# Optimization experiments

Hardware: AMD Instinct MI355X
Metric: run time of the kernel (lower is better)

## Reference

```python
import jax, jax.numpy as jnp
import numpy as np

B, L, D, DH = 4, 2048, 1024, 2048

def setup_inputs() -> dict:
    key = jax.random.key(0)
    ks = jax.random.split(key, 9)
    return {
        "x": jax.random.normal(ks[0], (B, L, D), jnp.float32),
        "W_in": jax.random.normal(ks[1], (DH, D), jnp.float32) / np.sqrt(D).astype(np.float32),
        "b_in": jnp.zeros((DH,), jnp.float32),
        "W_out": jax.random.normal(ks[2], (D, DH), jnp.float32) / np.sqrt(DH).astype(np.float32),
        "b_out": jnp.zeros((D,), jnp.float32),
        "phazor": jax.random.normal(ks[3], (DH, 2), jnp.float32),
        "phazor_init": jax.random.normal(ks[4], (DH, 2), jnp.float32),
        "last_conv_re": jax.random.normal(ks[5], (B, DH), jnp.float32),
        "last_conv_im": jax.random.normal(ks[6], (B, DH), jnp.float32),
    }

def reference(x, W_in, b_in, W_out, b_out, phazor, phazor_init, last_conv_re, last_conv_im):
    batch, length, _ = x.shape
    # linear_in, cast to float32 (already fp32 here)
    h = x @ W_in.T + b_in                                  # [B, L, DH]
    # view_as_complex of [DH, 2] params
    p = phazor[:, 0] + 1j * phazor[:, 1]                   # [DH]
    p0 = phazor_init[:, 0] + 1j * phazor_init[:, 1]        # [DH]
    pa = jnp.abs(p)
    p = p / pa * jnp.exp(-pa)                              # unit phase, exp(-|p|) magnitude
    # phazor_progression[t, c] = p[c] ** t
    prog = p[None, :] ** jnp.arange(length)[:, None]       # [L, DH] complex
    filt = prog * p0[None, :]                              # [L, DH]
    # FFT convolution with zero padding to 2L (linear convolution)
    ff = jnp.fft.fft(filt, n=2 * length, axis=0)           # [2L, DH]
    xf = jnp.fft.fft(h, n=2 * length, axis=1)              # [B, 2L, DH]
    conv = jnp.fft.ifft(ff[None] * xf, axis=1)[:, :length] # [B, L, DH]
    # add decayed contribution of past state (detached state)
    last = last_conv_re + 1j * last_conv_im                # [B, DH]
    conv_with_past = conv + last[:, None, :] * prog[None] * p[None, None, :]
    y = jax.nn.silu(conv_with_past.real)                   # back to real dtype
    return y @ W_out.T + b_out                             # [B, L, D]
```

## Files before the change

### kernel.cpp

```cpp
#include <hip/hip_runtime.h>
#include <math.h>

#define WS_B  4
#define WS_L  2048
#define WS_D  1024
#define WS_DH 2048
#define WS_M  (WS_B * WS_L)
#define NCH   32
#define CHUNK (WS_L / NCH)

typedef __attribute__((ext_vector_type(4))) float     f32x4;
typedef _Float16 f16x8 __attribute__((ext_vector_type(8)));
typedef _Float16 f16x4 __attribute__((ext_vector_type(4)));

#define GLDS(gptr, lptr) \
    __builtin_amdgcn_global_load_lds( \
        (const __attribute__((address_space(1))) unsigned int*)(gptr), \
        (__attribute__((address_space(3))) unsigned int*)(lptr), 16, 0, 0)

__global__ void pack_f16(const float* __restrict__ src, _Float16* __restrict__ dst,
                         int K, int k8log, int nChunks) {
    int chunk = blockIdx.x * 256 + threadIdx.x;
    if (chunk >= nChunks) return;
    int r    = chunk & 127;
    int rest = chunk >> 7;
    int K8m  = (1 << k8log) - 1;
    int kc   = rest & K8m;
    int rb   = rest >> k8log;
    const float* s = src + ((size_t)(rb * 128 + r) * K + kc * 8);
    f32x4 v0 = *(const f32x4*)s;
    f32x4 v1 = *(const f32x4*)(s + 4);
    f16x8 h;
#pragma unroll
    for (int k = 0; k < 4; ++k) { h[k] = (_Float16)v0[k]; h[4 + k] = (_Float16)v1[k]; }
    *(f16x8*)(dst + (size_t)chunk * 8) = h;
}

template<int K8, int LDC, typename OutT>
__global__ __launch_bounds__(256, 4)
void gemm_f16_packed(const _Float16* __restrict__ A, const _Float16* __restrict__ B,
                     const float* __restrict__ bias, OutT* __restrict__ C)
{
    __shared__ alignas(16) _Float16 sA[2][4][128][8];
    __shared__ alignas(16) _Float16 sB[2][4][128][8];

    const int tid  = threadIdx.x;
    const int lane = tid & 63;
    const int wave = tid >> 6;
    const int wm   = (wave >> 1) * 64;
    const int wn   = (wave & 1) * 64;
    const int m15  = lane & 15;
    const int q    = lane >> 4;

    const int bm = blockIdx.x;
    const int bn = blockIdx.y;

    f32x4 acc[4][4] = {};

    auto stage = [&](int kc0, int buf) {
#pragma unroll
        for (int i = 0; i < 2; ++i) {
            int c   = i * 256 + tid;
            int row = c & 127;
            int kq  = c >> 7;
            size_t ac = ((size_t)(bm * K8 + kc0 + kq) * 128 + row) * 8;
            size_t bc = ((size_t)(bn * K8 + kc0 + kq) * 128 + row) * 8;
            GLDS(A + ac, &sA[buf][kq][row][0]);
            GLDS(B + bc, &sB[buf][kq][row][0]);
        }
    };

    stage(0, 0);
    int buf = 0;
    for (int kc0 = 0; kc0 < K8; kc0 += 4, buf ^= 1) {
        __syncthreads();
        if (kc0 + 4 < K8) stage(kc0 + 4, buf ^ 1);

        f16x8 af[4], bf[4];
#pragma unroll
        for (int i = 0; i < 4; ++i) {
            af[i] = *(const f16x8*)&sA[buf][q][wm + i * 16 + m15][0];
            bf[i] = *(const f16x8*)&sB[buf][q][wn + i * 16 + m15][0];
        }
#pragma unroll
        for (int i = 0; i < 4; ++i)
#pragma unroll
            for (int j = 0; j < 4; ++j)
                acc[i][j] = __builtin_amdgcn_mfma_f32_16x16x32_f16(af[i], bf[j], acc[i][j], 0, 0, 0);
    }

    const int r4 = (lane >> 4) * 4;
#pragma unroll
    for (int j = 0; j < 4; ++j) {
        int col = bn * 128 + wn + j * 16 + m15;
        float bv = bias[col];
#pragma unroll
        for (int i = 0; i < 4; ++i) {
            int row0 = bm * 128 + wm + i * 16 + r4;
#pragma unroll
            for (int r = 0; r < 4; ++r)
                C[(size_t)(row0 + r) * LDC + col] = (OutT)(acc[i][j][r] + bv);
        }
    }
}

__device__ inline void compute_p(const float* __restrict__ phazor, int c, float& pre, float& pim) {
    float zr = phazor[2 * c], zi = phazor[2 * c + 1];
    float pa = sqrtf(zr * zr + zi * zi);
    float sc = expf(-pa) / pa;
    pre = zr * sc;
    pim = zi * sc;
}

__global__ void scan_local(const _Float16* __restrict__ h, const float* __restrict__ phazor,
                           const float* __restrict__ phazor_init, float* __restrict__ Uend) {
    int idx = blockIdx.x * blockDim.x + threadIdx.x;
    if (idx >= WS_B * NCH * WS_DH) return;
    int c  = idx & (WS_DH - 1);
    int bj = idx >> 11;
    int j  = bj & (NCH - 1);
    int b  = bj >> 5;
    float pre, pim;
    compute_p(phazor, c, pre, pim);
    float p0r = phazor_init[2 * c], p0i = phazor_init[2 * c + 1];
    const _Float16* hp = h + ((size_t)(b * WS_L + j * CHUNK)) * WS_DH + c;
    float ur = 0.f, ui = 0.f;
    for (int t = 0; t < CHUNK; t += 8) {
        float hv[8];
#pragma unroll
        for (int u = 0; u < 8; ++u) hv[u] = (float)hp[(size_t)(t + u) * WS_DH];
#pragma unroll
        for (int u = 0; u < 8; ++u) {
            float nr = fmaf(pre, ur, fmaf(-pim, ui, p0r * hv[u]));
            float ni = fmaf(pre, ui, fmaf( pim, ur, p0i * hv[u]));
            ur = nr; ui = ni;
        }
    }
    Uend[2 * idx] = ur;
    Uend[2 * idx + 1] = ui;
}

__global__ void scan_carry(const float* __restrict__ Uend, float* __restrict__ carry,
                           const float* __restrict__ phazor,
                           const float* __restrict__ last_re, const float* __restrict__ last_im) {
    int idx = blockIdx.x * blockDim.x + threadIdx.x;
    if (idx >= WS_B * WS_DH) return;
    int c = idx & (WS_DH - 1);
    int b = idx >> 11;
    float pre, pim;
    compute_p(phazor, c, pre, pim);
    float qr = pre, qi = pim;
#pragma unroll
    for (int s = 0; s < 6; ++s) {
        float nr = qr * qr - qi * qi;
        qi = 2.f * qr * qi;
        qr = nr;
    }
    float ur = last_re[idx], ui = last_im[idx];
    for (int j = 0; j < NCH; ++j) {
        int o = (b * NCH + j) * WS_DH + c;
        carry[2 * o] = ur;
        carry[2 * o + 1] = ui;
        float Lr = Uend[2 * o], Li = Uend[2 * o + 1];
        float nr = fmaf(qr, ur, fmaf(-qi, ui, Lr));
        float ni = fmaf(qr, ui, fmaf( qi, ur, Li));
        ur = nr; ui = ni;
    }
}

__global__ void scan_apply(const _Float16* __restrict__ h, const float* __restrict__ phazor,
                           const float* __restrict__ phazor_init, const float* __restrict__ carry,
                           _Float16* __restrict__ yh) {
    int idx = blockIdx.x * blockDim.x + threadIdx.x;
    if (idx >= WS_B * NCH * WS_DH) return;
    int c  = idx & (WS_DH - 1);
    int bj = idx >> 11;
    int j  = bj & (NCH - 1);
    int b  = bj >> 5;
    float pre, pim;
    compute_p(phazor, c, pre, pim);
    float p0r = phazor_init[2 * c], p0i = phazor_init[2 * c + 1];
    float ur = carry[2 * idx], ui = carry[2 * idx + 1];
    const int row0 = b * WS_L + j * CHUNK;
    const _Float16* hp = h + (size_t)row0 * WS_DH + c;
    const int chi = c >> 3, clo = c & 7;
    for (int t = 0; t < CHUNK; t += 8) {
        float hv[8];
#pragma unroll
        for (int u = 0; u < 8; ++u) hv[u] = (float)hp[(size_t)(t + u) * WS_DH];
#pragma unroll
        for (int u = 0; u < 8; ++u) {
            float nr = fmaf(pre, ur, fmaf(-pim, ui, p0r * hv[u]));
            float ni = fmaf(pre, ui, fmaf( pim, ur, p0i * hv[u]));
            ur = nr; ui = ni;
            float z  = ur;
            float yv = z / (1.f + expf(-z));
            int row = row0 + t + u;
            size_t o = (((size_t)(row >> 7) * 256 + chi) * 128 + (row & 127)) * 8 + clo;
            yh[o] = (_Float16)yv;
        }
    }
}

extern "C" void kernel_launch(void* const* d_in, const int* in_sizes, int n_in,
                              void* d_out, int out_size, void* d_ws, size_t ws_size,
                              hipStream_t stream)
{
    const float* x       = (const float*)d_in[0];
    const float* W_in    = (const float*)d_in[1];
    const float* b_in    = (const float*)d_in[2];
    const float* W_out   = (const float*)d_in[3];
    const float* b_out   = (const float*)d_in[4];
    const float* phazor  = (const float*)d_in[5];
    const float* ph_init = (const float*)d_in[6];
    const float* last_re = (const float*)d_in[7];
    const float* last_im = (const float*)d_in[8];
    float* out = (float*)d_out;

    char* ws = (char*)d_ws;
    size_t off = 0;
    auto alloc = [&](size_t bytes) {
        char* p = ws + off;
        off += (bytes + 255) & ~(size_t)255;
        return p;
    };
    _Float16* xp    = (_Float16*)alloc((size_t)WS_M * WS_D * 2);
    _Float16* w1p   = (_Float16*)alloc((size_t)WS_DH * WS_D * 2);
    _Float16* w2p   = (_Float16*)alloc((size_t)WS_D * WS_DH * 2);
    _Float16* h     = (_Float16*)alloc((size_t)WS_M * WS_DH * 2);
    _Float16* yhp   = (_Float16*)alloc((size_t)WS_M * WS_DH * 2);
    float*    Uend  = (float*)alloc((size_t)WS_B * NCH * WS_DH * 2 * 4);
    float*    carry = (float*)alloc((size_t)WS_B * NCH * WS_DH * 2 * 4);

    {
        int n = WS_M * WS_D / 8;
        pack_f16<<<dim3((n + 255) / 256), dim3(256), 0, stream>>>(x, xp, WS_D, 7, n);
        n = WS_DH * WS_D / 8;
        pack_f16<<<dim3((n + 255) / 256), dim3(256), 0, stream>>>(W_in, w1p, WS_D, 7, n);
        n = WS_D * WS_DH / 8;
        pack_f16<<<dim3((n + 255) / 256), dim3(256), 0, stream>>>(W_out, w2p, WS_DH, 8, n);
    }

    {
        dim3 g(WS_M / 128, WS_DH / 128);
        gemm_f16_packed<WS_D / 8, WS_DH, _Float16><<<g, dim3(256), 0, stream>>>(xp, w1p, b_in, h);
    }

    {
        int total = WS_B * NCH * WS_DH;
        scan_local<<<dim3(total / 256), dim3(256), 0, stream>>>(h, phazor, ph_init, Uend);
        scan_carry<<<dim3(WS_B * WS_DH / 256), dim3(256), 0, stream>>>(Uend, carry, phazor,
                                                                       last_re, last_im);
        scan_apply<<<dim3(total / 256), dim3(256), 0, stream>>>(h, phazor, ph_init, carry, yhp);
    }

    {
        dim3 g(WS_M / 128, WS_D / 128);
        gemm_f16_packed<WS_DH / 8, WS_D, float><<<g, dim3(256), 0, stream>>>(yhp, w2p, b_out, out);
    }
}
```

Measured before the change: 245.8 us.

## Vectorize scan over 8 channels, coalesce packing via LDS, deepen second GEMM K-tile

The scan kernels now handle 8 adjacent channels per thread with 16-byte loads and stores, and use 128 chunks instead of 32. The carry step's power-of-p loop and stores are adjusted to match. pack_f16 stages a 128x128 tile through LDS so that global reads are coalesced. The output GEMM uses a K-stage of 8 with a min-blocks hint of 2. The intent is to remove the strided 2-byte accesses in the scan and the uncoalesced packing reads, at the cost of more registers and a longer sequential carry loop.

```diff
diff --git a/kernel.cpp b/kernel.cpp
--- a/kernel.cpp
+++ b/kernel.cpp
@@ -6,8 +6,9 @@
 #define WS_D  1024
 #define WS_DH 2048
 #define WS_M  (WS_B * WS_L)
-#define NCH   32
+#define NCH   128
 #define CHUNK (WS_L / NCH)
+#define CB    8
 
 typedef __attribute__((ext_vector_type(4))) float     f32x4;
 typedef _Float16 f16x8 __attribute__((ext_vector_type(8)));
@@ -18,31 +19,45 @@
         (const __attribute__((address_space(1))) unsigned int*)(gptr), \
         (__attribute__((address_space(3))) unsigned int*)(lptr), 16, 0, 0)
 
-__global__ void pack_f16(const float* __restrict__ src, _Float16* __restrict__ dst,
-                         int K, int k8log, int nChunks) {
-    int chunk = blockIdx.x * 256 + threadIdx.x;
-    if (chunk >= nChunks) return;
-    int r    = chunk & 127;
-    int rest = chunk >> 7;
-    int K8m  = (1 << k8log) - 1;
-    int kc   = rest & K8m;
-    int rb   = rest >> k8log;
-    const float* s = src + ((size_t)(rb * 128 + r) * K + kc * 8);
-    f32x4 v0 = *(const f32x4*)s;
-    f32x4 v1 = *(const f32x4*)(s + 4);
-    f16x8 h;
-#pragma unroll
-    for (int k = 0; k < 4; ++k) { h[k] = (_Float16)v0[k]; h[4 + k] = (_Float16)v1[k]; }
-    *(f16x8*)(dst + (size_t)chunk * 8) = h;
-}
-
-template<int K8, int LDC, typename OutT>
-__global__ __launch_bounds__(256, 4)
+__global__ __launch_bounds__(256)
+void pack_f16(const float* __restrict__ src, _Float16* __restrict__ dst, int K) {
+    __shared__ alignas(16) _Float16 sT[128][136];
+    const int tid = threadIdx.x;
+    const int rb  = blockIdx.x;
+    const int kb  = blockIdx.y;
+    const int K8  = K >> 3;
+
+#pragma unroll
+    for (int it = 0; it < 16; ++it) {
+        int f    = it * 256 + tid;
+        int row  = f >> 5;
+        int col  = (f & 31) * 4;
+        f32x4 v  = *(const f32x4*)(src + (size_t)(rb * 128 + row) * K + kb * 128 + col);
+        f16x4 hv;
+#pragma unroll
+        for (int k = 0; k < 4; ++k) hv[k] = (_Float16)v[k];
+        *(f16x4*)&sT[row][col] = hv;
+    }
+    __syncthreads();
+
+#pragma unroll
+    for (int it = 0; it < 8; ++it) {
+        int c2 = it * 256 + tid;
+        int r  = c2 & 127;
+        int kq = c2 >> 7;
+        f16x8 hv = *(const f16x8*)&sT[r][kq * 8];
+        size_t chunk = ((size_t)rb * K8 + kb * 16 + kq) * 128 + r;
+        *(f16x8*)(dst + chunk * 8) = hv;
+    }
+}
+
+template<int K8, int LDC, int KQ, int MINB, typename OutT>
+__global__ __launch_bounds__(256, MINB)
 void gemm_f16_packed(const _Float16* __restrict__ A, const _Float16* __restrict__ B,
                      const float* __restrict__ bias, OutT* __restrict__ C)
 {
-    __shared__ alignas(16) _Float16 sA[2][4][128][8];
-    __shared__ alignas(16) _Float16 sB[2][4][128][8];
+    __shared__ alignas(16) _Float16 sA[2][KQ][128][8];
+    __shared__ alignas(16) _Float16 sB[2][KQ][128][8];
 
     const int tid  = threadIdx.x;
     const int lane = tid & 63;
@@ -59,7 +74,7 @@
 
     auto stage = [&](int kc0, int buf) {
 #pragma unroll
-        for (int i = 0; i < 2; ++i) {
+        for (int i = 0; i < KQ / 2; ++i) {
             int c   = i * 256 + tid;
             int row = c & 127;
             int kq  = c >> 7;
@@ -72,21 +87,24 @@
 
     stage(0, 0);
     int buf = 0;
-    for (int kc0 = 0; kc0 < K8; kc0 += 4, buf ^= 1) {
+    for (int kc0 = 0; kc0 < K8; kc0 += KQ, buf ^= 1) {
         __syncthreads();
-        if (kc0 + 4 < K8) stage(kc0 + 4, buf ^ 1);
-
-        f16x8 af[4], bf[4];
-#pragma unroll
-        for (int i = 0; i < 4; ++i) {
-            af[i] = *(const f16x8*)&sA[buf][q][wm + i * 16 + m15][0];
-            bf[i] = *(const f16x8*)&sB[buf][q][wn + i * 16 + m15][0];
-        }
-#pragma unroll
-        for (int i = 0; i < 4; ++i)
-#pragma unroll
-            for (int j = 0; j < 4; ++j)
-                acc[i][j] = __builtin_amdgcn_mfma_f32_16x16x32_f16(af[i], bf[j], acc[i][j], 0, 0, 0);
+        if (kc0 + KQ < K8) stage(kc0 + KQ, buf ^ 1);
+
+#pragma unroll
+        for (int kk = 0; kk < KQ / 4; ++kk) {
+            f16x8 af[4], bf[4];
+#pragma unroll
+            for (int i = 0; i < 4; ++i) {
+                af[i] = *(const f16x8*)&sA[buf][kk * 4 + q][wm + i * 16 + m15][0];
+                bf[i] = *(const f16x8*)&sB[buf][kk * 4 + q][wn + i * 16 + m15][0];
+            }
+#pragma unroll
+            for (int i = 0; i < 4; ++i)
+#pragma unroll
+                for (int j = 0; j < 4; ++j)
+                    acc[i][j] = __builtin_amdgcn_mfma_f32_16x16x32_f16(af[i], bf[j], acc[i][j], 0, 0, 0);
+        }
     }
 
     const int r4 = (lane >> 4) * 4;
@@ -115,29 +133,35 @@
 __global__ void scan_local(const _Float16* __restrict__ h, const float* __restrict__ phazor,
                            const float* __restrict__ phazor_init, float* __restrict__ Uend) {
     int idx = blockIdx.x * blockDim.x + threadIdx.x;
-    if (idx >= WS_B * NCH * WS_DH) return;
-    int c  = idx & (WS_DH - 1);
-    int bj = idx >> 11;
-    int j  = bj & (NCH - 1);
-    int b  = bj >> 5;
-    float pre, pim;
-    compute_p(phazor, c, pre, pim);
-    float p0r = phazor_init[2 * c], p0i = phazor_init[2 * c + 1];
-    const _Float16* hp = h + ((size_t)(b * WS_L + j * CHUNK)) * WS_DH + c;
-    float ur = 0.f, ui = 0.f;
-    for (int t = 0; t < CHUNK; t += 8) {
-        float hv[8];
-#pragma unroll
-        for (int u = 0; u < 8; ++u) hv[u] = (float)hp[(size_t)(t + u) * WS_DH];
-#pragma unroll
-        for (int u = 0; u < 8; ++u) {
-            float nr = fmaf(pre, ur, fmaf(-pim, ui, p0r * hv[u]));
-            float ni = fmaf(pre, ui, fmaf( pim, ur, p0i * hv[u]));
-            ur = nr; ui = ni;
-        }
-    }
-    Uend[2 * idx] = ur;
-    Uend[2 * idx + 1] = ui;
+    int cb   = idx & (WS_DH / CB - 1);
+    int rest = idx >> 8;
+    int j    = rest & (NCH - 1);
+    int b    = rest >> 7;
+    int c0   = cb * CB;
+    float pre[CB], pim[CB], p0r[CB], p0i[CB], ur[CB] = {}, ui[CB] = {};
+#pragma unroll
+    for (int u = 0; u < CB; ++u) {
+        compute_p(phazor, c0 + u, pre[u], pim[u]);
+        p0r[u] = phazor_init[2 * (c0 + u)];
+        p0i[u] = phazor_init[2 * (c0 + u) + 1];
+    }
+    const int row0 = b * WS_L + j * CHUNK;
+    const _Float16* hp = h + (size_t)row0 * WS_DH + c0;
+#pragma unroll
+    for (int t = 0; t < CHUNK; ++t) {
+        f16x8 v = *(const f16x8*)(hp + (size_t)t * WS_DH);
+#pragma unroll
+        for (int u = 0; u < CB; ++u) {
+            float hv = (float)v[u];
+            float nr = fmaf(pre[u], ur[u], fmaf(-pim[u], ui[u], p0r[u] * hv));
+            float ni = fmaf(pre[u], ui[u], fmaf( pim[u], ur[u], p0i[u] * hv));
+            ur[u] = nr; ui[u] = ni;
+        }
+    }
+    float2* Ue = (float2*)Uend;
+    size_t o = ((size_t)(b * NCH + j)) * WS_DH + c0;
+#pragma unroll
+    for (int u = 0; u < CB; ++u) { float2 w; w.x = ur[u]; w.y = ui[u]; Ue[o + u] = w; }
 }
 
 __global__ void scan_carry(const float* __restrict__ Uend, float* __restrict__ carry,
@@ -151,19 +175,22 @@
     compute_p(phazor, c, pre, pim);
     float qr = pre, qi = pim;
 #pragma unroll
-    for (int s = 0; s < 6; ++s) {
+    for (int s = 0; s < 4; ++s) {
         float nr = qr * qr - qi * qi;
         qi = 2.f * qr * qi;
         qr = nr;
     }
     float ur = last_re[idx], ui = last_im[idx];
+    const float2* Ue = (const float2*)Uend;
+    float2* Ca = (float2*)carry;
+#pragma unroll 4
     for (int j = 0; j < NCH; ++j) {
-        int o = (b * NCH + j) * WS_DH + c;
-        carry[2 * o] = ur;
-        carry[2 * o + 1] = ui;
-        float Lr = Uend[2 * o], Li = Uend[2 * o + 1];
-        float nr = fmaf(qr, ur, fmaf(-qi, ui, Lr));
-        float ni = fmaf(qr, ui, fmaf( qi, ur, Li));
+        size_t o = (size_t)(b * NCH + j) * WS_DH + c;
+        float2 w; w.x = ur; w.y = ui;
+        Ca[o] = w;
+        float2 L = Ue[o];
+        float nr = fmaf(qr, ur, fmaf(-qi, ui, L.x));
+        float ni = fmaf(qr, ui, fmaf( qi, ur, L.y));
         ur = nr; ui = ni;
     }
 }
@@ -172,33 +199,40 @@
                            const float* __restrict__ phazor_init, const float* __restrict__ carry,
                            _Float16* __restrict__ yh) {
     int idx = blockIdx.x * blockDim.x + threadIdx.x;
-    if (idx >= WS_B * NCH * WS_DH) return;
-    int c  = idx & (WS_DH - 1);
-    int bj = idx >> 11;
-    int j  = bj & (NCH - 1);
-    int b  = bj >> 5;
-    float pre, pim;
-    compute_p(phazor, c, pre, pim);
-    float p0r = phazor_init[2 * c], p0i = phazor_init[2 * c + 1];
-    float ur = carry[2 * idx], ui = carry[2 * idx + 1];
+    int cb   = idx & (WS_DH / CB - 1);
+    int rest = idx >> 8;
+    int j    = rest & (NCH - 1);
+    int b    = rest >> 7;
+    int c0   = cb * CB;
+    float pre[CB], pim[CB], p0r[CB], p0i[CB], ur[CB], ui[CB];
+    const float2* Ca = (const float2*)carry;
+    size_t co = ((size_t)(b * NCH + j)) * WS_DH + c0;
+#pragma unroll
+    for (int u = 0; u < CB; ++u) {
+        compute_p(phazor, c0 + u, pre[u], pim[u]);
+        p0r[u] = phazor_init[2 * (c0 + u)];
+        p0i[u] = phazor_init[2 * (c0 + u) + 1];
+        float2 w = Ca[co + u];
+        ur[u] = w.x; ui[u] = w.y;
+    }
     const int row0 = b * WS_L + j * CHUNK;
-    const _Float16* hp = h + (size_t)row0 * WS_DH + c;
-    const int chi = c >> 3, clo = c & 7;
-    for (int t = 0; t < CHUNK; t += 8) {
-        float hv[8];
-#pragma unroll
-        for (int u = 0; u < 8; ++u) hv[u] = (float)hp[(size_t)(t + u) * WS_DH];
-#pragma unroll
-        for (int u = 0; u < 8; ++u) {
-            float nr = fmaf(pre, ur, fmaf(-pim, ui, p0r * hv[u]));
-            float ni = fmaf(pre, ui, fmaf( pim, ur, p0i * hv[u]));
-            ur = nr; ui = ni;
-            float z  = ur;
-            float yv = z / (1.f + expf(-z));
-            int row = row0 + t + u;
-            size_t o = (((size_t)(row >> 7) * 256 + chi) * 128 + (row & 127)) * 8 + clo;
-            yh[o] = (_Float16)yv;
-        }
+    const _Float16* hp = h + (size_t)row0 * WS_DH + c0;
+#pragma unroll
+    for (int t = 0; t < CHUNK; ++t) {
+        f16x8 v = *(const f16x8*)(hp + (size_t)t * WS_DH);
+        f16x8 yv;
+#pragma unroll
+        for (int u = 0; u < CB; ++u) {
+            float hv = (float)v[u];
+            float nr = fmaf(pre[u], ur[u], fmaf(-pim[u], ui[u], p0r[u] * hv));
+            float ni = fmaf(pre[u], ui[u], fmaf( pim[u], ur[u], p0i[u] * hv));
+            ur[u] = nr; ui[u] = ni;
+            float z = nr;
+            yv[u] = (_Float16)(z / (1.f + expf(-z)));
+        }
+        int row = row0 + t;
+        size_t o = ((size_t)(row >> 7) * 256 + cb) * 128 + (row & 127);
+        *(f16x8*)(yh + o * 8) = yv;
     }
 }
 
@@ -232,22 +266,17 @@
     float*    Uend  = (float*)alloc((size_t)WS_B * NCH * WS_DH * 2 * 4);
     float*    carry = (float*)alloc((size_t)WS_B * NCH * WS_DH * 2 * 4);
 
-    {
-        int n = WS_M * WS_D / 8;
-        pack_f16<<<dim3((n + 255) / 256), dim3(256), 0, stream>>>(x, xp, WS_D, 7, n);
-        n = WS_DH * WS_D / 8;
-        pack_f16<<<dim3((n + 255) / 256), dim3(256), 0, stream>>>(W_in, w1p, WS_D, 7, n);
-        n = WS_D * WS_DH / 8;
-        pack_f16<<<dim3((n + 255) / 256), dim3(256), 0, stream>>>(W_out, w2p, WS_DH, 8, n);
-    }
+    pack_f16<<<dim3(WS_M / 128, WS_D / 128),  dim3(256), 0, stream>>>(x,     xp,  WS_D);
+    pack_f16<<<dim3(WS_DH / 128, WS_D / 128), dim3(256), 0, stream>>>(W_in,  w1p, WS_D);
+    pack_f16<<<dim3(WS_D / 128, WS_DH / 128), dim3(256), 0, stream>>>(W_out, w2p, WS_DH);
 
     {
         dim3 g(WS_M / 128, WS_DH / 128);
-        gemm_f16_packed<WS_D / 8, WS_DH, _Float16><<<g, dim3(256), 0, stream>>>(xp, w1p, b_in, h);
+        gemm_f16_packed<WS_D / 8, WS_DH, 4, 4, _Float16><<<g, dim3(256), 0, stream>>>(xp, w1p, b_in, h);
     }
 
     {
-        int total = WS_B * NCH * WS_DH;
+        int total = WS_B * NCH * WS_DH / CB;
         scan_local<<<dim3(total / 256), dim3(256), 0, stream>>>(h, phazor, ph_init, Uend);
         scan_carry<<<dim3(WS_B * WS_DH / 256), dim3(256), 0, stream>>>(Uend, carry, phazor,
                                                                        last_re, last_im);
@@ -256,6 +285,6 @@
 
     {
         dim3 g(WS_M / 128, WS_D / 128);
-        gemm_f16_packed<WS_DH / 8, WS_D, float><<<g, dim3(256), 0, stream>>>(yhp, w2p, b_out, out);
-    }
-}
+        gemm_f16_packed<WS_DH / 8, WS_D, 8, 2, float><<<g, dim3(256), 0, stream>>>(yhp, w2p, b_out, out);
+    }
+}
```

Result: slower. 262.8 us (+6.9%).
